# Kernel optimization log

Hardware: AMD Instinct MI355X
Metric: run time of the kernel (lower is better)

Reference implementation:

```python
import jax, jax.numpy as jnp
import numpy as np

EMBED_DIM = 1024
NUM_HEADS = 16
HEAD_DIM = EMBED_DIM // NUM_HEADS
SCALE = HEAD_DIM ** -0.5


def setup_inputs() -> dict:
    key = jax.random.key(0)
    k_x, k_wqkv, k_bqkv, k_wp, k_bp = jax.random.split(key, 5)
    B, N = 2, 2048
    x = jax.random.normal(k_x, (B, N, EMBED_DIM), dtype=jnp.float32)
    # torch.nn.Linear default init: U(-1/sqrt(fan_in), 1/sqrt(fan_in))
    lim = 1.0 / np.sqrt(EMBED_DIM)
    W_qkv = jax.random.uniform(k_wqkv, (EMBED_DIM, 3 * EMBED_DIM), jnp.float32, -lim, lim)
    b_qkv = jax.random.uniform(k_bqkv, (3 * EMBED_DIM,), jnp.float32, -lim, lim)
    W_proj = jax.random.uniform(k_wp, (EMBED_DIM, EMBED_DIM), jnp.float32, -lim, lim)
    b_proj = jax.random.uniform(k_bp, (EMBED_DIM,), jnp.float32, -lim, lim)
    return {"x": x, "W_qkv": W_qkv, "b_qkv": b_qkv, "W_proj": W_proj, "b_proj": b_proj}


def reference(x, W_qkv, b_qkv, W_proj, b_proj):
    B, N, C = x.shape
    qkv = x @ W_qkv + b_qkv                              # [B, N, 3C]
    qkv = qkv.reshape(B, N, 3, NUM_HEADS, HEAD_DIM)
    qkv = jnp.transpose(qkv, (2, 0, 3, 1, 4))            # [3, B, H, N, D]
    q, k, v = qkv[0], qkv[1], qkv[2]
    attn = jnp.einsum('bhnd,bhmd->bhnm', q, k) * SCALE   # [B, H, N, N]
    attn = jax.nn.softmax(attn, axis=-1)
    out = jnp.einsum('bhnm,bhmd->bhnd', attn, v)         # [B, H, N, D]
    out = jnp.transpose(out, (0, 2, 1, 3)).reshape(B, N, C)
    return out @ W_proj + b_proj
```

## Files before the change

### kernel.cpp

```cpp
#include <hip/hip_runtime.h>
#include <math.h>

typedef unsigned short u16;
typedef _Float16 f16;
typedef f16 f16x8 __attribute__((ext_vector_type(8)));
typedef __fp16 hp16x2 __attribute__((ext_vector_type(2)));
typedef float f32x4 __attribute__((ext_vector_type(4)));
typedef float f32x16 __attribute__((ext_vector_type(16)));
typedef unsigned u32x2 __attribute__((ext_vector_type(2)));

#define SEQ   2048
#define NH    16
#define HD    64
#define EMB   1024
#define NQKV  3072
#define BATCH 2
#define QSCALE 0.18033688f

__device__ __forceinline__ u16 f2h(float f) {
  union { f16 h; u16 u; } w; w.h = (f16)f; return w.u;
}

__device__ __forceinline__ void gload16(const void* g, void* l) {
  __builtin_amdgcn_global_load_lds(
      (const __attribute__((address_space(1))) unsigned int*)g,
      (__attribute__((address_space(3))) unsigned int*)l, 16, 0, 0);
}

__device__ __forceinline__ void cvt_wt_tile(const float* __restrict__ W,
                                            u16* __restrict__ Wt,
                                            int K, int N, int n0, int k0, int t) {
  __shared__ u16 T[64][68];
  const int rr = t >> 4, cc = (t & 15) << 2;
#pragma unroll
  for (int p = 0; p < 4; p++) {
    const int kr = p * 16 + rr;
    float4 v = *reinterpret_cast<const float4*>(&W[(size_t)(k0 + kr) * N + n0 + cc]);
    T[cc + 0][kr] = f2h(v.x); T[cc + 1][kr] = f2h(v.y);
    T[cc + 2][kr] = f2h(v.z); T[cc + 3][kr] = f2h(v.w);
  }
  __syncthreads();
#pragma unroll
  for (int p = 0; p < 4; p++) {
    const int nr = p * 16 + rr;
    union { u16 s[4]; unsigned long long d; } o;
    o.s[0] = T[nr][cc + 0]; o.s[1] = T[nr][cc + 1];
    o.s[2] = T[nr][cc + 2]; o.s[3] = T[nr][cc + 3];
    *reinterpret_cast<unsigned long long*>(&Wt[(size_t)(n0 + nr) * K + k0 + cc]) = o.d;
  }
}

__global__ __launch_bounds__(256) void k_pre(const float* __restrict__ X,
                                             u16* __restrict__ Xh,
                                             const float* __restrict__ Wqkv,
                                             u16* __restrict__ Wt,
                                             const float* __restrict__ Wproj,
                                             u16* __restrict__ Wpt) {
  const int b = blockIdx.x;
  const int t = threadIdx.x;
  if (b < 2048) {
    const size_t i = ((size_t)b * 256 + t) * 8;
    float4 a = *reinterpret_cast<const float4*>(&X[i]);
    float4 c = *reinterpret_cast<const float4*>(&X[i + 4]);
    union { hp16x2 h2[4]; float4 f; } pk;
    pk.h2[0] = __builtin_amdgcn_cvt_pkrtz(a.x, a.y);
    pk.h2[1] = __builtin_amdgcn_cvt_pkrtz(a.z, a.w);
    pk.h2[2] = __builtin_amdgcn_cvt_pkrtz(c.x, c.y);
    pk.h2[3] = __builtin_amdgcn_cvt_pkrtz(c.z, c.w);
    *reinterpret_cast<float4*>(&Xh[i]) = pk.f;
  } else if (b < 2048 + 768) {
    const int id = b - 2048;
    cvt_wt_tile(Wqkv, Wt, EMB, NQKV, (id % 48) << 6, (id / 48) << 6, t);
  } else {
    const int id = b - 2816;
    cvt_wt_tile(Wproj, Wpt, EMB, EMB, (id % 16) << 6, (id / 16) << 6, t);
  }
}

__device__ __forceinline__ void gemm_core(const u16* __restrict__ Ag,
                                          const u16* __restrict__ Bg,
                                          int m0, int n0, int t,
                                          f32x4 acc[4][4]) {
  __shared__ __align__(16) u16 As[128 * 32];
  __shared__ __align__(16) u16 Bs[128 * 32];
  const int lane = t & 63, w = t >> 6;
  const int l15  = lane & 15, quad = lane >> 4;
  const int wm = w >> 1, wn = w & 1;
  const int srow  = lane >> 2;
  const int gslot = (lane & 3) ^ ((srow >> 1) & 3);
  const int xk    = (quad ^ ((l15 >> 1) & 3)) << 3;

  for (int k0 = 0; k0 < EMB; k0 += 32) {
    __syncthreads();
#pragma unroll
    for (int i = 0; i < 2; i++) {
      const int ca = w * 2 + i;
      const int arow = ca * 16 + srow;
      gload16(Ag + (size_t)(m0 + arow) * EMB + k0 + gslot * 8, &As[ca * 512]);
      gload16(Bg + (size_t)(n0 + arow) * EMB + k0 + gslot * 8, &Bs[ca * 512]);
    }
    __syncthreads();
    f16x8 af[4], bf[4];
#pragma unroll
    for (int s = 0; s < 4; s++)
      af[s] = *reinterpret_cast<const f16x8*>(&As[(wm * 64 + s * 16 + l15) * 32 + xk]);
#pragma unroll
    for (int s = 0; s < 4; s++)
      bf[s] = *reinterpret_cast<const f16x8*>(&Bs[(wn * 64 + s * 16 + l15) * 32 + xk]);
#pragma unroll
    for (int i = 0; i < 4; i++)
#pragma unroll
      for (int j = 0; j < 4; j++)
        acc[i][j] = __builtin_amdgcn_mfma_f32_16x16x32_f16(af[i], bf[j], acc[i][j], 0, 0, 0);
  }
}

__global__ __launch_bounds__(256) void k_qkv(const u16* __restrict__ Ag,
                                             const u16* __restrict__ Bg,
                                             const float* __restrict__ bias,
                                             u16* __restrict__ qo,
                                             u16* __restrict__ ko,
                                             u16* __restrict__ vo) {
  const int t = threadIdx.x;
  const int lane = t & 63, w = t >> 6;
  const int l15 = lane & 15, quad = lane >> 4;
  const int wm = w >> 1, wn = w & 1;
  const int m0 = blockIdx.y << 7, n0 = blockIdx.x << 7;
  f32x4 acc[4][4];
#pragma unroll
  for (int i = 0; i < 4; i++)
#pragma unroll
    for (int j = 0; j < 4; j++) acc[i][j] = (f32x4){0.f, 0.f, 0.f, 0.f};
  gemm_core(Ag, Bg, m0, n0, t, acc);
#pragma unroll
  for (int j = 0; j < 4; j++) {
    const int c = n0 + wn * 64 + j * 16 + l15;
    const int which = c >> 10, h = (c >> 6) & 15, d = c & 63;
    const float bv = bias[c];
    const float sc = (which == 0) ? QSCALE : 1.0f;
#pragma unroll
    for (int i = 0; i < 4; i++) {
#pragma unroll
      for (int r = 0; r < 4; r++) {
        const int m  = m0 + wm * 64 + i * 16 + quad * 4 + r;
        const int bb = m >> 11, n = m & (SEQ - 1);
        const u16 val = f2h((acc[i][j][r] + bv) * sc);
        if (which == 2)
          vo[(((size_t)bb * NH + h) * HD + d) * SEQ + n] = val;
        else if (which == 1)
          ko[((((size_t)bb * NH + h) * SEQ) + n) * HD + d] = val;
        else
          qo[((((size_t)bb * NH + h) * SEQ) + n) * HD + d] = val;
      }
    }
  }
}

__global__ __launch_bounds__(256) void k_proj(const u16* __restrict__ Ag,
                                              const u16* __restrict__ Bg,
                                              const float* __restrict__ bias,
                                              float* __restrict__ out) {
  const int t = threadIdx.x;
  const int lane = t & 63, w = t >> 6;
  const int l15 = lane & 15, quad = lane >> 4;
  const int wm = w >> 1, wn = w & 1;
  const int m0 = blockIdx.y << 7, n0 = blockIdx.x << 7;
  f32x4 acc[4][4];
#pragma unroll
  for (int i = 0; i < 4; i++)
#pragma unroll
    for (int j = 0; j < 4; j++) acc[i][j] = (f32x4){0.f, 0.f, 0.f, 0.f};
  gemm_core(Ag, Bg, m0, n0, t, acc);
#pragma unroll
  for (int j = 0; j < 4; j++) {
    const int c = n0 + wn * 64 + j * 16 + l15;
    const float bv = bias[c];
#pragma unroll
    for (int i = 0; i < 4; i++) {
#pragma unroll
      for (int r = 0; r < 4; r++) {
        const int m = m0 + wm * 64 + i * 16 + quad * 4 + r;
        out[(size_t)m * EMB + c] = acc[i][j][r] + bv;
      }
    }
  }
}

__global__ __launch_bounds__(512, 4) void k_attn(const u16* __restrict__ Qg,
                                                 const u16* __restrict__ Kg,
                                                 const u16* __restrict__ Vtg,
                                                 u16* __restrict__ AO) {
  __shared__ __align__(16) u16 KV[2][2][2][64 * 64];
  __shared__ float Lx[256];
  const int t    = threadIdx.x;
  const int lane = t & 63, w = t >> 6;
  const int grp  = w >> 2, wl = w & 3;
  const int l31  = lane & 31, hi = lane >> 5;
  const int id   = blockIdx.y * 16 + blockIdx.x;
  const int swz  = ((id & 7) << 6) | (id >> 3);
  const int bh   = swz >> 4;
  const int q0   = (swz & 15) << 7;
  const size_t base = (size_t)bh * SEQ * HD;

  f16x8 qf[4];
  {
    const u16* qp = Qg + base + (size_t)(q0 + 32 * wl + l31) * HD + hi * 8;
#pragma unroll
    for (int c = 0; c < 4; c++) {
      union { float4 f; f16x8 v; } fu;
      fu.f = *reinterpret_cast<const float4*>(qp + c * 16);
      qf[c] = fu.v;
    }
  }

  f32x16 O0 = {}, O1 = {};
  float lsum = 0.f;
  const int fsw = (l31 >> 1) & 7;
  const int srw = lane >> 3, ssl = lane & 7;
  const int kbeg = grp << 10;
  const int kend = kbeg + (SEQ / 2);

  auto STAGE = [&](int buf, int kt) {
    u16* Ksb = KV[buf][grp][0];
    u16* Vsb = KV[buf][grp][1];
#pragma unroll
    for (int i = 0; i < 2; i++) {
      const int ca  = wl * 2 + i;
      const int row = ca * 8 + srw;
      const int sg  = (ssl ^ ((row >> 1) & 7)) << 3;
      gload16(Kg  + base + (size_t)(kt + row) * HD + sg, &Ksb[ca * 512]);
      gload16(Vtg + base + (size_t)row * SEQ + kt + sg,  &Vsb[ca * 512]);
    }
  };

  STAGE(0, kbeg);
  __syncthreads();

  int cur = 0;
  for (int kt = kbeg; kt < kend; kt += 64) {
    if (kt + 64 < kend) STAGE(cur ^ 1, kt + 64);
    const u16* Ks = KV[cur][grp][0];
    const u16* Vs = KV[cur][grp][1];

#pragma unroll
    for (int sk = 0; sk < 2; sk++) {
      f32x16 c = {};
      __builtin_amdgcn_s_setprio(1);
#pragma unroll
      for (int cc = 0; cc < 4; cc++) {
        f16x8 kf = *reinterpret_cast<const f16x8*>(
            &Ks[(sk * 32 + l31) * 64 + (((cc * 2 + hi) ^ fsw) << 3)]);
        c = __builtin_amdgcn_mfma_f32_32x32x16_f16(kf, qf[cc], c, 0, 0, 0);
      }
      __builtin_amdgcn_s_setprio(0);
      unsigned pw[4][2];
#pragma unroll
      for (int g = 0; g < 4; g++) {
        const float p0 = __builtin_amdgcn_exp2f(c[4 * g + 0]);
        const float p1 = __builtin_amdgcn_exp2f(c[4 * g + 1]);
        const float p2 = __builtin_amdgcn_exp2f(c[4 * g + 2]);
        const float p3 = __builtin_amdgcn_exp2f(c[4 * g + 3]);
        lsum += (p0 + p1) + (p2 + p3);
        union { hp16x2 h; unsigned u; } w0, w1;
        w0.h = __builtin_amdgcn_cvt_pkrtz(p0, p1);
        w1.h = __builtin_amdgcn_cvt_pkrtz(p2, p3);
        pw[g][0] = w0.u; pw[g][1] = w1.u;
      }
      __builtin_amdgcn_s_setprio(1);
#pragma unroll
      for (int s = 0; s < 2; s++) {
        u32x2 r02 = __builtin_amdgcn_permlane32_swap(
            pw[2 * s][0], pw[2 * s + 1][0], false, false);
        u32x2 r13 = __builtin_amdgcn_permlane32_swap(
            pw[2 * s][1], pw[2 * s + 1][1], false, false);
        union { unsigned u[4]; f16x8 v; } fr;
        fr.u[0] = r02.x;
        fr.u[1] = r13.x;
        fr.u[2] = r02.y;
        fr.u[3] = r13.y;
        const int cc = sk * 2 + s;
        f16x8 vf0 = *reinterpret_cast<const f16x8*>(
            &Vs[l31 * 64 + (((cc * 2 + hi) ^ fsw) << 3)]);
        f16x8 vf1 = *reinterpret_cast<const f16x8*>(
            &Vs[(32 + l31) * 64 + (((cc * 2 + hi) ^ fsw) << 3)]);
        O0 = __builtin_amdgcn_mfma_f32_32x32x16_f16(fr.v, vf0, O0, 0, 0, 0);
        O1 = __builtin_amdgcn_mfma_f32_32x32x16_f16(fr.v, vf1, O1, 0, 0, 0);
      }
      __builtin_amdgcn_s_setprio(0);
    }
    __syncthreads();
    cur ^= 1;
  }

  float* Xch = reinterpret_cast<float*>(&KV[0][0][0][0]);
  const int li = wl * 64 + lane;
  if (grp == 1) {
#pragma unroll
    for (int g4 = 0; g4 < 4; g4++) {
      f32x4 v0 = { O0[4 * g4 + 0], O0[4 * g4 + 1], O0[4 * g4 + 2], O0[4 * g4 + 3] };
      *reinterpret_cast<f32x4*>(&Xch[(g4 * 256 + li) * 4]) = v0;
      f32x4 v1 = { O1[4 * g4 + 0], O1[4 * g4 + 1], O1[4 * g4 + 2], O1[4 * g4 + 3] };
      *reinterpret_cast<f32x4*>(&Xch[((4 + g4) * 256 + li) * 4]) = v1;
    }
    Lx[li] = lsum;
  }
  __syncthreads();
  if (grp == 0) {
#pragma unroll
    for (int g4 = 0; g4 < 4; g4++) {
      f32x4 v0 = *reinterpret_cast<const f32x4*>(&Xch[(g4 * 256 + li) * 4]);
      f32x4 v1 = *reinterpret_cast<const f32x4*>(&Xch[((4 + g4) * 256 + li) * 4]);
#pragma unroll
      for (int j = 0; j < 4; j++) {
        O0[4 * g4 + j] += v0[j];
        O1[4 * g4 + j] += v1[j];
      }
    }
    lsum += Lx[li];
    lsum += __shfl_xor(lsum, 32);
    const int b = bh >> 4, h = bh & 15;
#pragma unroll
    for (int g = 0; g < 4; g++) {
#pragma unroll
      for (int rr = 0; rr < 4; rr++) {
        const int r = g * 4 + rr;
        const int qrow = rr + 8 * g + 4 * hi;
        const float inv = 1.f / __shfl(lsum, qrow, 64);
        const int n = q0 + 32 * wl + qrow;
        u16* dst = AO + ((size_t)(b * SEQ + n)) * EMB + h * HD;
        dst[l31]      = f2h(O0[r] * inv);
        dst[32 + l31] = f2h(O1[r] * inv);
      }
    }
  }
}

extern "C" void kernel_launch(void* const* d_in, const int* in_sizes, int n_in,
                              void* d_out, int out_size, void* d_ws, size_t ws_size,
                              hipStream_t stream) {
  (void)in_sizes; (void)n_in; (void)out_size; (void)ws_size;
  const float* x     = (const float*)d_in[0];
  const float* Wqkv  = (const float*)d_in[1];
  const float* bqkv  = (const float*)d_in[2];
  const float* Wproj = (const float*)d_in[3];
  const float* bproj = (const float*)d_in[4];
  float* out = (float*)d_out;

  const size_t NE = (size_t)BATCH * SEQ * EMB;
  u16* q    = (u16*)d_ws;
  u16* k    = q + NE;
  u16* vt   = k + NE;
  u16* aoxh = vt + NE;
  u16* Wt   = aoxh + NE;
  u16* Wpt  = Wt + (size_t)NQKV * EMB;

  k_pre<<<3072, 256, 0, stream>>>(x, aoxh, Wqkv, Wt, Wproj, Wpt);

  dim3 gq(NQKV / 128, (BATCH * SEQ) / 128);
  k_qkv<<<gq, 256, 0, stream>>>(aoxh, Wt, bqkv, q, k, vt);

  dim3 ga(SEQ / 128, BATCH * NH);
  k_attn<<<ga, 512, 0, stream>>>(q, k, vt, aoxh);

  dim3 gp(EMB / 128, (BATCH * SEQ) / 128);
  k_proj<<<gp, 256, 0, stream>>>(aoxh, Wpt, bproj, out);
}
```

Before: 193.5 us.

## Double-buffer GEMM LDS tiles and remap blocks for XCD-local L2 reuse

The shared GEMM core now uses two LDS buffers so the global-to-LDS load of the next K tile is issued before the MFMAs on the current one, with one barrier per iteration instead of two. MFMA sections get raised wave priority. The QKV and projection kernels remap block IDs so that blocks landing on the same XCD cover a contiguous region of M/N tiles, which should improve L2 reuse of A and B. The cost is doubled LDS use per block, which may reduce occupancy.

New measurement: 200.2 us. 1.03x slower.

```diff
diff --git a/kernel.cpp b/kernel.cpp
--- a/kernel.cpp
+++ b/kernel.cpp
@@ -81,8 +81,8 @@
                                           const u16* __restrict__ Bg,
                                           int m0, int n0, int t,
                                           f32x4 acc[4][4]) {
-  __shared__ __align__(16) u16 As[128 * 32];
-  __shared__ __align__(16) u16 Bs[128 * 32];
+  __shared__ __align__(16) u16 As[2][128 * 32];
+  __shared__ __align__(16) u16 Bs[2][128 * 32];
   const int lane = t & 63, w = t >> 6;
   const int l15  = lane & 15, quad = lane >> 4;
   const int wm = w >> 1, wn = w & 1;
@@ -90,28 +90,38 @@
   const int gslot = (lane & 3) ^ ((srow >> 1) & 3);
   const int xk    = (quad ^ ((l15 >> 1) & 3)) << 3;
 
-  for (int k0 = 0; k0 < EMB; k0 += 32) {
-    __syncthreads();
+  auto STAGE = [&](int buf, int k0) {
 #pragma unroll
     for (int i = 0; i < 2; i++) {
       const int ca = w * 2 + i;
       const int arow = ca * 16 + srow;
-      gload16(Ag + (size_t)(m0 + arow) * EMB + k0 + gslot * 8, &As[ca * 512]);
-      gload16(Bg + (size_t)(n0 + arow) * EMB + k0 + gslot * 8, &Bs[ca * 512]);
-    }
-    __syncthreads();
+      gload16(Ag + (size_t)(m0 + arow) * EMB + k0 + gslot * 8, &As[buf][ca * 512]);
+      gload16(Bg + (size_t)(n0 + arow) * EMB + k0 + gslot * 8, &Bs[buf][ca * 512]);
+    }
+  };
+
+  STAGE(0, 0);
+  __syncthreads();
+
+  for (int kt = 0; kt < EMB / 32; ++kt) {
+    if (kt + 1 < EMB / 32) STAGE((kt + 1) & 1, (kt + 1) * 32);
+    const u16* Asb = As[kt & 1];
+    const u16* Bsb = Bs[kt & 1];
     f16x8 af[4], bf[4];
 #pragma unroll
     for (int s = 0; s < 4; s++)
-      af[s] = *reinterpret_cast<const f16x8*>(&As[(wm * 64 + s * 16 + l15) * 32 + xk]);
+      af[s] = *reinterpret_cast<const f16x8*>(&Asb[(wm * 64 + s * 16 + l15) * 32 + xk]);
 #pragma unroll
     for (int s = 0; s < 4; s++)
-      bf[s] = *reinterpret_cast<const f16x8*>(&Bs[(wn * 64 + s * 16 + l15) * 32 + xk]);
+      bf[s] = *reinterpret_cast<const f16x8*>(&Bsb[(wn * 64 + s * 16 + l15) * 32 + xk]);
+    __builtin_amdgcn_s_setprio(1);
 #pragma unroll
     for (int i = 0; i < 4; i++)
 #pragma unroll
       for (int j = 0; j < 4; j++)
         acc[i][j] = __builtin_amdgcn_mfma_f32_16x16x32_f16(af[i], bf[j], acc[i][j], 0, 0, 0);
+    __builtin_amdgcn_s_setprio(0);
+    __syncthreads();
   }
 }
 
@@ -125,7 +135,11 @@
   const int lane = t & 63, w = t >> 6;
   const int l15 = lane & 15, quad = lane >> 4;
   const int wm = w >> 1, wn = w & 1;
-  const int m0 = blockIdx.y << 7, n0 = blockIdx.x << 7;
+  const int id  = blockIdx.y * 24 + blockIdx.x;
+  const int xcd = id & 7, r = id >> 3;
+  const int n_t = 12 * (xcd & 1) + r % 12;
+  const int m_t = 8 * (xcd >> 1) + r / 12;
+  const int m0 = m_t << 7, n0 = n_t << 7;
   f32x4 acc[4][4];
 #pragma unroll
   for (int i = 0; i < 4; i++)
@@ -141,10 +155,10 @@
 #pragma unroll
     for (int i = 0; i < 4; i++) {
 #pragma unroll
-      for (int r = 0; r < 4; r++) {
-        const int m  = m0 + wm * 64 + i * 16 + quad * 4 + r;
+      for (int r2 = 0; r2 < 4; r2++) {
+        const int m  = m0 + wm * 64 + i * 16 + quad * 4 + r2;
         const int bb = m >> 11, n = m & (SEQ - 1);
-        const u16 val = f2h((acc[i][j][r] + bv) * sc);
+        const u16 val = f2h((acc[i][j][r2] + bv) * sc);
         if (which == 2)
           vo[(((size_t)bb * NH + h) * HD + d) * SEQ + n] = val;
         else if (which == 1)
@@ -164,7 +178,11 @@
   const int lane = t & 63, w = t >> 6;
   const int l15 = lane & 15, quad = lane >> 4;
   const int wm = w >> 1, wn = w & 1;
-  const int m0 = blockIdx.y << 7, n0 = blockIdx.x << 7;
+  const int id  = blockIdx.y * 8 + blockIdx.x;
+  const int xcd = id & 7, r = id >> 3;
+  const int n_t = 4 * (xcd & 1) + (r & 3);
+  const int m_t = 8 * (xcd >> 1) + (r >> 2);
+  const int m0 = m_t << 7, n0 = n_t << 7;
   f32x4 acc[4][4];
 #pragma unroll
   for (int i = 0; i < 4; i++)
@@ -178,9 +196,9 @@
 #pragma unroll
     for (int i = 0; i < 4; i++) {
 #pragma unroll
-      for (int r = 0; r < 4; r++) {
-        const int m = m0 + wm * 64 + i * 16 + quad * 4 + r;
-        out[(size_t)m * EMB + c] = acc[i][j][r] + bv;
+      for (int r2 = 0; r2 < 4; r2++) {
+        const int m = m0 + wm * 64 + i * 16 + quad * 4 + r2;
+        out[(size_t)m * EMB + c] = acc[i][j][r2] + bv;
       }
     }
   }
```
